# Performance work log

Measured on AMD Instinct MI355X. Metric: run time of the kernel, lower is better.

The kernel has to match this reference:

```python
import jax, jax.numpy as jnp
import numpy as np

B, S, D_IN, D_OUT = 4, 4096, 2048, 2048


def setup_inputs() -> dict:
    key = jax.random.key(0)
    kx, kw = jax.random.split(key)
    x = jax.random.normal(kx, (B, S, D_IN), dtype=jnp.float32)
    weight = jax.random.normal(kw, (D_OUT, D_IN), dtype=jnp.float32) * 0.02
    return {"x": x, "weight": weight}


def reference(x, weight):
    # Per-row absmax int8 activation quantization
    x_scale = jnp.clip(jnp.max(jnp.abs(x), axis=-1, keepdims=True), 1e-05, None)  # [B,S,1]
    x_quant = jnp.clip(jnp.round(x / x_scale * 127.0), -128.0, 127.0)
    # Ternary weight quantization (mean-centered absmean scale)
    w_mean = jnp.mean(weight)
    w_centered = weight - w_mean
    w_scale = jnp.clip(jnp.mean(jnp.abs(w_centered)), 1e-05, None)
    w_quant = jnp.clip(jnp.round(w_centered / w_scale), -1.0, 1.0)
    # GEMM on quantized values, then dequant rescale
    y = jnp.einsum('bsi,oi->bso', x_quant, w_quant)  # [B,S,D_OUT]
    y = y * (w_scale * x_scale / 127.0)
    return y.astype(x.dtype)
```

## Files before the change

### kernel.cpp

```cpp
#include <hip/hip_runtime.h>
#include <stdint.h>

#define M_TOT 16384
#define K_DIM 2048
#define N_DIM 2048
#define W_ELEMS (N_DIM * K_DIM)

typedef int v4i  __attribute__((ext_vector_type(4)));

__device__ __forceinline__ void async_load16(const void* gptr, void* lptr) {
    __builtin_amdgcn_global_load_lds(
        (__attribute__((address_space(1))) void*)(uintptr_t)gptr,
        (__attribute__((address_space(3))) void*)(uint32_t)(uintptr_t)lptr,
        16, 0, 0);
}

__device__ __forceinline__ int qclamp(float v, int lo, int hi) {
    int q = (int)rintf(v);
    q = q > hi ? hi : (q < lo ? lo : q);
    return q & 255;
}

__global__ __launch_bounds__(256) void wsum_kernel(const float* __restrict__ w,
                                                   double* __restrict__ spart) {
    int tid = blockIdx.x * 256 + threadIdx.x;
    const float4* w4 = (const float4*)w;
    double s = 0.0;
    #pragma unroll
    for (int it = 0; it < 8; it++) {
        float4 v = w4[tid + it * 131072];
        s += (double)v.x + (double)v.y + (double)v.z + (double)v.w;
    }
    #pragma unroll
    for (int off = 32; off; off >>= 1) s += __shfl_down(s, off);
    __shared__ double ls[4];
    if ((threadIdx.x & 63) == 0) ls[threadIdx.x >> 6] = s;
    __syncthreads();
    if (threadIdx.x == 0) spart[blockIdx.x] = ls[0] + ls[1] + ls[2] + ls[3];
}

__global__ __launch_bounds__(256) void wabs_kernel(const float* __restrict__ w,
                                                   const double* __restrict__ spart,
                                                   double* __restrict__ apart) {
    __shared__ double ls[4];
    double sm = spart[threadIdx.x] + spart[threadIdx.x + 256];
    #pragma unroll
    for (int off = 32; off; off >>= 1) sm += __shfl_down(sm, off);
    if ((threadIdx.x & 63) == 0) ls[threadIdx.x >> 6] = sm;
    __syncthreads();
    double mean = (ls[0] + ls[1] + ls[2] + ls[3]) * (1.0 / (double)W_ELEMS);
    __syncthreads();
    int tid = blockIdx.x * 256 + threadIdx.x;
    const float4* w4 = (const float4*)w;
    double s = 0.0;
    #pragma unroll
    for (int it = 0; it < 8; it++) {
        float4 v = w4[tid + it * 131072];
        s += fabs((double)v.x - mean) + fabs((double)v.y - mean) +
             fabs((double)v.z - mean) + fabs((double)v.w - mean);
    }
    #pragma unroll
    for (int off = 32; off; off >>= 1) s += __shfl_down(s, off);
    if ((threadIdx.x & 63) == 0) ls[threadIdx.x >> 6] = s;
    __syncthreads();
    if (threadIdx.x == 0) apart[blockIdx.x] = ls[0] + ls[1] + ls[2] + ls[3];
}

__global__ __launch_bounds__(256) void quant_kernel(
    const float* __restrict__ x, const float* __restrict__ w,
    const double* __restrict__ spart, const double* __restrict__ apart,
    int8_t* __restrict__ xq, int8_t* __restrict__ wq,
    float* __restrict__ xscale, float* __restrict__ wsf)
{
    const int t = threadIdx.x;
    if (blockIdx.x < 4096) {
        const int row  = (blockIdx.x << 2) | (t >> 6);
        const int lane = t & 63;
        const float4* xr = (const float4*)(x + (size_t)row * K_DIM);
        float4 v[8];
        #pragma unroll
        for (int i = 0; i < 8; i++) v[i] = xr[lane + (i << 6)];
        float m = 0.0f;
        #pragma unroll
        for (int i = 0; i < 8; i++)
            m = fmaxf(m, fmaxf(fmaxf(fabsf(v[i].x), fabsf(v[i].y)),
                               fmaxf(fabsf(v[i].z), fabsf(v[i].w))));
        #pragma unroll
        for (int off = 32; off; off >>= 1) m = fmaxf(m, __shfl_xor(m, off));
        const float scale = fmaxf(m, 1e-5f);
        if (lane == 0) xscale[row] = scale;
        const float rs = 127.0f / scale;
        int* outp = (int*)(xq + (size_t)row * K_DIM);
        #pragma unroll
        for (int i = 0; i < 8; i++) {
            int p = qclamp(v[i].x * rs, -128, 127)
                  | (qclamp(v[i].y * rs, -128, 127) << 8)
                  | (qclamp(v[i].z * rs, -128, 127) << 16)
                  | (qclamp(v[i].w * rs, -128, 127) << 24);
            outp[lane + (i << 6)] = p;
        }
    } else {
        __shared__ double ls0[4], ls1[4];
        double s0 = spart[t] + spart[t + 256];
        double s1 = apart[t] + apart[t + 256];
        #pragma unroll
        for (int off = 32; off; off >>= 1) {
            s0 += __shfl_down(s0, off);
            s1 += __shfl_down(s1, off);
        }
        if ((t & 63) == 0) { ls0[t >> 6] = s0; ls1[t >> 6] = s1; }
        __syncthreads();
        float mean  = (float)((ls0[0] + ls0[1] + ls0[2] + ls0[3]) * (1.0 / (double)W_ELEMS));
        float scale = (float)fmax((ls1[0] + ls1[1] + ls1[2] + ls1[3]) * (1.0 / (double)W_ELEMS), 1e-5);
        const float ri = 1.0f / scale;
        int i = (blockIdx.x - 4096) * 256 + t;
        float4 v = ((const float4*)w)[i];
        int p = qclamp((v.x - mean) * ri, -1, 1)
              | (qclamp((v.y - mean) * ri, -1, 1) << 8)
              | (qclamp((v.z - mean) * ri, -1, 1) << 16)
              | (qclamp((v.w - mean) * ri, -1, 1) << 24);
        ((int*)wq)[i] = p;
        if (i == 0) wsf[0] = scale * (1.0f / 127.0f);
    }
}

__global__ __launch_bounds__(512, 2) void gemm_i8_kernel(
    const int8_t* __restrict__ xq, const int8_t* __restrict__ wq,
    const float* __restrict__ xscale, const float* __restrict__ wsf,
    float* __restrict__ out)
{
    __shared__ __align__(16) int8_t lsA[3][16384];
    __shared__ __align__(16) int8_t lsB[3][16384];

    const int tid  = threadIdx.x;
    const int lane = tid & 63;
    const int wv   = tid >> 6;

    const int flat = blockIdx.x;
    const int nf   = ((flat & 7) << 6) | (flat >> 3);
    const int bm   = nf >> 3;
    const int bn   = nf & 7;

    const int sChunk = (((tid & 3) ^ ((tid >> 3) & 3)) << 4);
    const int8_t* gAb = xq + (size_t)(bm * 256 + (tid >> 2)) * K_DIM + sChunk;
    const int8_t* gBb = wq + (size_t)(bn * 256 + (tid >> 2)) * K_DIM + sChunk;

    #define STAGE(NB, T)                                                       \
        do {                                                                   \
            async_load16(gAb + ((T) << 6),                       lsA[NB] + tid * 16); \
            async_load16(gAb + ((T) << 6) + (size_t)128 * K_DIM, lsA[NB] + 8192 + tid * 16); \
            async_load16(gBb + ((T) << 6),                       lsB[NB] + tid * 16); \
            async_load16(gBb + ((T) << 6) + (size_t)128 * K_DIM, lsB[NB] + 8192 + tid * 16); \
        } while (0)

    const int wm = (wv >> 2) << 7;
    const int wn = (wv & 3) << 6;
    const int fr = lane & 15;
    const int fc = lane >> 4;
    int aoff[8], boff[4];
    #pragma unroll
    for (int mi = 0; mi < 8; mi++) {
        int ra = wm + mi * 16 + fr;
        aoff[mi] = ra * 64 + ((fc ^ ((ra >> 1) & 3)) << 4);
    }
    #pragma unroll
    for (int nj = 0; nj < 4; nj++) {
        int rb = wn + nj * 16 + fr;
        boff[nj] = rb * 64 + ((fc ^ ((rb >> 1) & 3)) << 4);
    }

    v4i acc[8][4] = {};

    #define COMPUTE(CB)                                                        \
        do {                                                                   \
            v4i af[8], bf[4];                                                  \
            _Pragma("unroll")                                                  \
            for (int mi_ = 0; mi_ < 8; mi_++)                                  \
                af[mi_] = *(const v4i*)(lsA[CB] + aoff[mi_]);                  \
            _Pragma("unroll")                                                  \
            for (int nj_ = 0; nj_ < 4; nj_++)                                  \
                bf[nj_] = *(const v4i*)(lsB[CB] + boff[nj_]);                  \
            __builtin_amdgcn_s_setprio(1);                                     \
            _Pragma("unroll")                                                  \
            for (int mi_ = 0; mi_ < 8; mi_++)                                  \
                _Pragma("unroll")                                              \
                for (int nj_ = 0; nj_ < 4; nj_++)                              \
                    acc[mi_][nj_] = __builtin_amdgcn_mfma_i32_16x16x64_i8(     \
                        af[mi_], bf[nj_], acc[mi_][nj_], 0, 0, 0);             \
            __builtin_amdgcn_s_setprio(0);                                     \
        } while (0)

    #define TILE_MID(CB, NB, T)                                                \
        do {                                                                   \
            STAGE(NB, (T) + 2);                                                \
            COMPUTE(CB);                                                       \
            asm volatile("s_waitcnt vmcnt(4)" ::: "memory");                   \
            __builtin_amdgcn_s_barrier();                                      \
        } while (0)

    STAGE(0, 0);
    STAGE(1, 1);
    asm volatile("s_waitcnt vmcnt(4)" ::: "memory");
    __builtin_amdgcn_s_barrier();

    for (int tt = 0; tt < 30; tt += 3) {
        TILE_MID(0, 2, tt);
        TILE_MID(1, 0, tt + 1);
        TILE_MID(2, 1, tt + 2);
    }
    COMPUTE(0);
    asm volatile("s_waitcnt vmcnt(0)" ::: "memory");
    __builtin_amdgcn_s_barrier();
    COMPUTE(1);

    #undef TILE_MID
    #undef COMPUTE
    #undef STAGE

    const float f127 = wsf[0];
    #pragma unroll
    for (int mi = 0; mi < 8; mi++) {
        #pragma unroll
        for (int rg = 0; rg < 4; rg++) {
            const int mg = bm * 256 + wm + mi * 16 + (lane >> 4) * 4 + rg;
            const float fs = f127 * xscale[mg];
            float* orow = out + (size_t)mg * N_DIM + bn * 256 + wn;
            #pragma unroll
            for (int nj = 0; nj < 4; nj++)
                orow[nj * 16 + fr] = fs * (float)acc[mi][nj][rg];
        }
    }
}

extern "C" void kernel_launch(void* const* d_in, const int* in_sizes, int n_in,
                              void* d_out, int out_size, void* d_ws, size_t ws_size,
                              hipStream_t stream) {
    const float* x = (const float*)d_in[0];
    const float* w = (const float*)d_in[1];
    float* out = (float*)d_out;

    char* ws = (char*)d_ws;
    double* spart  = (double*)ws;
    double* apart  = (double*)(ws + 4096);
    float*  wsf    = (float*)(ws + 8192);
    float*  xscale = (float*)(ws + 12288);
    int8_t* xq     = (int8_t*)(ws + 12288 + 65536);
    int8_t* wq     = xq + (size_t)M_TOT * K_DIM;

    wsum_kernel <<<512, 256, 0, stream>>>(w, spart);
    wabs_kernel <<<512, 256, 0, stream>>>(w, spart, apart);
    quant_kernel<<<8192, 256, 0, stream>>>(x, w, spart, apart, xq, wq, xscale, wsf);
    gemm_i8_kernel<<<512, 512, 0, stream>>>(xq, wq, xscale, wsf, out);
}
```

Baseline: 307.9 us.

## Fuse weight stats and quantization into one cooperative kernel with grid syncs

Replaces the three preprocessing kernels (weight sum, weight abs-deviation, quantize) with a single cooperative kernel of 1024 blocks that uses grid-wide syncs between the reduction phases, then quantizes weights and activations. This removes two kernel launches and their inter-kernel gaps. The tradeoffs are grid-sync overhead, 1024 resident blocks limiting occupancy for the x-quant phase, and weights being read three times. It also switches reciprocal multiplies to divisions to match reference rounding.

```diff
diff --git a/kernel.cpp b/kernel.cpp
--- a/kernel.cpp
+++ b/kernel.cpp
@@ -1,5 +1,8 @@
 #include <hip/hip_runtime.h>
+#include <hip/hip_cooperative_groups.h>
 #include <stdint.h>
+
+namespace cg = cooperative_groups;
 
 #define M_TOT 16384
 #define K_DIM 2048
@@ -21,61 +24,78 @@
     return q & 255;
 }
 
-__global__ __launch_bounds__(256) void wsum_kernel(const float* __restrict__ w,
-                                                   double* __restrict__ spart) {
-    int tid = blockIdx.x * 256 + threadIdx.x;
-    const float4* w4 = (const float4*)w;
-    double s = 0.0;
-    #pragma unroll
-    for (int it = 0; it < 8; it++) {
-        float4 v = w4[tid + it * 131072];
-        s += (double)v.x + (double)v.y + (double)v.z + (double)v.w;
-    }
-    #pragma unroll
-    for (int off = 32; off; off >>= 1) s += __shfl_down(s, off);
-    __shared__ double ls[4];
-    if ((threadIdx.x & 63) == 0) ls[threadIdx.x >> 6] = s;
-    __syncthreads();
-    if (threadIdx.x == 0) spart[blockIdx.x] = ls[0] + ls[1] + ls[2] + ls[3];
-}
-
-__global__ __launch_bounds__(256) void wabs_kernel(const float* __restrict__ w,
-                                                   const double* __restrict__ spart,
-                                                   double* __restrict__ apart) {
-    __shared__ double ls[4];
-    double sm = spart[threadIdx.x] + spart[threadIdx.x + 256];
-    #pragma unroll
-    for (int off = 32; off; off >>= 1) sm += __shfl_down(sm, off);
-    if ((threadIdx.x & 63) == 0) ls[threadIdx.x >> 6] = sm;
-    __syncthreads();
-    double mean = (ls[0] + ls[1] + ls[2] + ls[3]) * (1.0 / (double)W_ELEMS);
-    __syncthreads();
-    int tid = blockIdx.x * 256 + threadIdx.x;
-    const float4* w4 = (const float4*)w;
-    double s = 0.0;
-    #pragma unroll
-    for (int it = 0; it < 8; it++) {
-        float4 v = w4[tid + it * 131072];
-        s += fabs((double)v.x - mean) + fabs((double)v.y - mean) +
-             fabs((double)v.z - mean) + fabs((double)v.w - mean);
-    }
-    #pragma unroll
-    for (int off = 32; off; off >>= 1) s += __shfl_down(s, off);
-    if ((threadIdx.x & 63) == 0) ls[threadIdx.x >> 6] = s;
-    __syncthreads();
-    if (threadIdx.x == 0) apart[blockIdx.x] = ls[0] + ls[1] + ls[2] + ls[3];
-}
-
-__global__ __launch_bounds__(256) void quant_kernel(
+__global__ __launch_bounds__(256, 4) void pre_kernel(
     const float* __restrict__ x, const float* __restrict__ w,
-    const double* __restrict__ spart, const double* __restrict__ apart,
+    double* __restrict__ spart, double* __restrict__ apart,
     int8_t* __restrict__ xq, int8_t* __restrict__ wq,
     float* __restrict__ xscale, float* __restrict__ wsf)
 {
-    const int t = threadIdx.x;
-    if (blockIdx.x < 4096) {
-        const int row  = (blockIdx.x << 2) | (t >> 6);
-        const int lane = t & 63;
+    const int t  = threadIdx.x;
+    const int b  = blockIdx.x;
+    const int gt = b * 256 + t;
+    const float4* w4 = (const float4*)w;
+    __shared__ double ls[4];
+
+    double s = 0.0;
+    #pragma unroll
+    for (int i = 0; i < 4; i++) {
+        float4 v = w4[gt + i * 262144];
+        s += (double)v.x + (double)v.y + (double)v.z + (double)v.w;
+    }
+    #pragma unroll
+    for (int off = 32; off; off >>= 1) s += __shfl_down(s, off);
+    if ((t & 63) == 0) ls[t >> 6] = s;
+    __syncthreads();
+    if (t == 0) spart[b] = ls[0] + ls[1] + ls[2] + ls[3];
+    cg::this_grid().sync();
+
+    double sm = spart[t] + spart[t + 256] + spart[t + 512] + spart[t + 768];
+    #pragma unroll
+    for (int off = 32; off; off >>= 1) sm += __shfl_down(sm, off);
+    __syncthreads();
+    if ((t & 63) == 0) ls[t >> 6] = sm;
+    __syncthreads();
+    const double mean = (ls[0] + ls[1] + ls[2] + ls[3]) * (1.0 / (double)W_ELEMS);
+    double a = 0.0;
+    #pragma unroll
+    for (int i = 0; i < 4; i++) {
+        float4 v = w4[gt + i * 262144];
+        a += fabs((double)v.x - mean) + fabs((double)v.y - mean) +
+             fabs((double)v.z - mean) + fabs((double)v.w - mean);
+    }
+    #pragma unroll
+    for (int off = 32; off; off >>= 1) a += __shfl_down(a, off);
+    __syncthreads();
+    if ((t & 63) == 0) ls[t >> 6] = a;
+    __syncthreads();
+    if (t == 0) apart[b] = ls[0] + ls[1] + ls[2] + ls[3];
+    cg::this_grid().sync();
+
+    double am = apart[t] + apart[t + 256] + apart[t + 512] + apart[t + 768];
+    #pragma unroll
+    for (int off = 32; off; off >>= 1) am += __shfl_down(am, off);
+    __syncthreads();
+    if ((t & 63) == 0) ls[t >> 6] = am;
+    __syncthreads();
+    const float wscale = (float)fmax(
+        (ls[0] + ls[1] + ls[2] + ls[3]) * (1.0 / (double)W_ELEMS), 1e-5);
+    const float fmean = (float)mean;
+    if (b == 0 && t == 0) wsf[0] = wscale * (1.0f / 127.0f);
+
+    #pragma unroll
+    for (int i = 0; i < 4; i++) {
+        const int f = gt + i * 262144;
+        float4 v = w4[f];
+        int p = qclamp((v.x - fmean) / wscale, -1, 1)
+              | (qclamp((v.y - fmean) / wscale, -1, 1) << 8)
+              | (qclamp((v.z - fmean) / wscale, -1, 1) << 16)
+              | (qclamp((v.w - fmean) / wscale, -1, 1) << 24);
+        ((int*)wq)[f] = p;
+    }
+
+    const int wv = t >> 6, lane = t & 63;
+    for (int it = 0; it < 4; it++) {
+        const int row = (b << 4) + (wv << 2) + it;
         const float4* xr = (const float4*)(x + (size_t)row * K_DIM);
         float4 v[8];
         #pragma unroll
@@ -89,38 +109,15 @@
         for (int off = 32; off; off >>= 1) m = fmaxf(m, __shfl_xor(m, off));
         const float scale = fmaxf(m, 1e-5f);
         if (lane == 0) xscale[row] = scale;
-        const float rs = 127.0f / scale;
         int* outp = (int*)(xq + (size_t)row * K_DIM);
         #pragma unroll
         for (int i = 0; i < 8; i++) {
-            int p = qclamp(v[i].x * rs, -128, 127)
-                  | (qclamp(v[i].y * rs, -128, 127) << 8)
-                  | (qclamp(v[i].z * rs, -128, 127) << 16)
-                  | (qclamp(v[i].w * rs, -128, 127) << 24);
+            int p = qclamp(v[i].x / scale * 127.0f, -128, 127)
+                  | (qclamp(v[i].y / scale * 127.0f, -128, 127) << 8)
+                  | (qclamp(v[i].z / scale * 127.0f, -128, 127) << 16)
+                  | (qclamp(v[i].w / scale * 127.0f, -128, 127) << 24);
             outp[lane + (i << 6)] = p;
         }
-    } else {
-        __shared__ double ls0[4], ls1[4];
-        double s0 = spart[t] + spart[t + 256];
-        double s1 = apart[t] + apart[t + 256];
-        #pragma unroll
-        for (int off = 32; off; off >>= 1) {
-            s0 += __shfl_down(s0, off);
-            s1 += __shfl_down(s1, off);
-        }
-        if ((t & 63) == 0) { ls0[t >> 6] = s0; ls1[t >> 6] = s1; }
-        __syncthreads();
-        float mean  = (float)((ls0[0] + ls0[1] + ls0[2] + ls0[3]) * (1.0 / (double)W_ELEMS));
-        float scale = (float)fmax((ls1[0] + ls1[1] + ls1[2] + ls1[3]) * (1.0 / (double)W_ELEMS), 1e-5);
-        const float ri = 1.0f / scale;
-        int i = (blockIdx.x - 4096) * 256 + t;
-        float4 v = ((const float4*)w)[i];
-        int p = qclamp((v.x - mean) * ri, -1, 1)
-              | (qclamp((v.y - mean) * ri, -1, 1) << 8)
-              | (qclamp((v.z - mean) * ri, -1, 1) << 16)
-              | (qclamp((v.w - mean) * ri, -1, 1) << 24);
-        ((int*)wq)[i] = p;
-        if (i == 0) wsf[0] = scale * (1.0f / 127.0f);
     }
 }
 
@@ -147,10 +144,10 @@
 
     #define STAGE(NB, T)                                                       \
         do {                                                                   \
-            async_load16(gAb + ((T) << 6),                       lsA[NB] + tid * 16); \
-            async_load16(gAb + ((T) << 6) + (size_t)128 * K_DIM, lsA[NB] + 8192 + tid * 16); \
-            async_load16(gBb + ((T) << 6),                       lsB[NB] + tid * 16); \
-            async_load16(gBb + ((T) << 6) + (size_t)128 * K_DIM, lsB[NB] + 8192 + tid * 16); \
+            async_load16(gAb + ((size_t)(T) << 6),                       lsA[NB] + tid * 16); \
+            async_load16(gAb + ((size_t)(T) << 6) + (size_t)128 * K_DIM, lsA[NB] + 8192 + tid * 16); \
+            async_load16(gBb + ((size_t)(T) << 6),                       lsB[NB] + tid * 16); \
+            async_load16(gBb + ((size_t)(T) << 6) + (size_t)128 * K_DIM, lsB[NB] + 8192 + tid * 16); \
         } while (0)
 
     const int wm = (wv >> 2) << 7;
@@ -241,14 +238,15 @@
 
     char* ws = (char*)d_ws;
     double* spart  = (double*)ws;
-    double* apart  = (double*)(ws + 4096);
-    float*  wsf    = (float*)(ws + 8192);
-    float*  xscale = (float*)(ws + 12288);
-    int8_t* xq     = (int8_t*)(ws + 12288 + 65536);
+    double* apart  = (double*)(ws + 8192);
+    float*  wsf    = (float*)(ws + 16384);
+    float*  xscale = (float*)(ws + 20480);
+    int8_t* xq     = (int8_t*)(ws + 20480 + 65536);
     int8_t* wq     = xq + (size_t)M_TOT * K_DIM;
 
-    wsum_kernel <<<512, 256, 0, stream>>>(w, spart);
-    wabs_kernel <<<512, 256, 0, stream>>>(w, spart, apart);
-    quant_kernel<<<8192, 256, 0, stream>>>(x, w, spart, apart, xq, wq, xscale, wsf);
+    void* args[] = {(void*)&x, (void*)&w, (void*)&spart, (void*)&apart,
+                    (void*)&xq, (void*)&wq, (void*)&xscale, (void*)&wsf};
+    hipLaunchCooperativeKernel((void*)pre_kernel, dim3(1024), dim3(256),
+                               args, 0, stream);
     gemm_i8_kernel<<<512, 512, 0, stream>>>(xq, wq, xscale, wsf, out);
 }
```

Result: slower. 494.0 us (+60.5%).
